# Kernel optimization log

Hardware: AMD Instinct MI355X
Metric: run time of the kernel (lower is better)

## Reference

```python
import jax, jax.numpy as jnp
import numpy as np

RANGE_MIN = -5.0
RANGE_MAX = 5.0
MIN_BIN_SIZE = 1e-4
MIN_SLOPE = 1e-4
N = 33554432  # 32M elements, memory-bound
K = 8         # number of bins -> params has 3*K + 1 = 25 entries


def setup_inputs() -> dict:
    key = jax.random.key(0)
    kx, kp = jax.random.split(key)
    x = jax.random.normal(kx, (N,), dtype=jnp.float32)
    params = jax.random.normal(kp, (3 * K + 1,), dtype=jnp.float32)
    return {"x": x, "params": params}


def _normalize_params(params):
    k = (params.shape[-1] - 1) // 3
    widths_unnorm = params[:k]
    heights_unnorm = params[k:2 * k]
    slopes_unnorm = params[2 * k:]
    total_size = RANGE_MAX - RANGE_MIN
    widths = jax.nn.softmax(widths_unnorm, axis=-1) * (total_size - k * MIN_BIN_SIZE) + MIN_BIN_SIZE
    heights = jax.nn.softmax(heights_unnorm, axis=-1) * (total_size - k * MIN_BIN_SIZE) + MIN_BIN_SIZE
    slopes_offset = jnp.log(jnp.exp(1.0 - MIN_SLOPE) - 1.0)
    slopes = jax.nn.softplus(slopes_unnorm + slopes_offset) + MIN_SLOPE
    x_pos = jnp.concatenate([jnp.array([0.0], dtype=params.dtype), jnp.cumsum(widths)]) + RANGE_MIN
    y_pos = jnp.concatenate([jnp.array([0.0], dtype=params.dtype), jnp.cumsum(heights)]) + RANGE_MIN
    return x_pos, y_pos, slopes


def reference(x, params):
    x_pos, y_pos, slopes = _normalize_params(params)
    below_range = x < RANGE_MIN
    above_range = x > RANGE_MAX
    slope_left, slope_right = slopes[0], slopes[-1]
    y_linear_left = (x - RANGE_MIN) * slope_left + RANGE_MIN
    y_linear_right = (x - RANGE_MAX) * slope_right + RANGE_MAX
    logdet_linear_left = jnp.log(slope_left)
    logdet_linear_right = jnp.log(slope_right)

    num_bins = x_pos.shape[-1] - 1
    bin_idx = jnp.searchsorted(x_pos[1:-1], x, side='right')
    bin_idx = jnp.clip(bin_idx, 0, num_bins - 1)
    x_k, x_k1 = x_pos[bin_idx], x_pos[bin_idx + 1]
    y_k, y_k1 = y_pos[bin_idx], y_pos[bin_idx + 1]
    slope_k, slope_k1 = slopes[bin_idx], slopes[bin_idx + 1]

    width = x_k1 - x_k
    height = y_k1 - y_k
    xi = jnp.clip((x - x_k) / width, 0.0, 1.0)
    s = height / width
    numerator = s * xi * xi + slope_k * xi * (1.0 - xi)
    denominator = s + (slope_k1 + slope_k - 2.0 * s) * xi * (1.0 - xi)
    y_spline = y_k + height * numerator / denominator

    xi_1m = 1.0 - xi
    xi_xi_1m = xi * xi_1m
    num_derivative = s * s * (slope_k1 * xi * xi + 2.0 * s * xi_xi_1m + slope_k * xi_1m * xi_1m)
    derivative = num_derivative / (denominator * denominator)
    logdet_spline = jnp.log(derivative)

    y = jnp.where(below_range, y_linear_left, jnp.where(above_range, y_linear_right, y_spline))
    logdet = jnp.where(below_range, logdet_linear_left, jnp.where(above_range, logdet_linear_right, logdet_spline))
    return (y, logdet)
```

## Files before the change

kernel.cpp:

```cpp
#include <hip/hip_runtime.h>
#include <math.h>

#define KBINS 8
#define R_MIN -5.0f
#define R_MAX 5.0f
#define MIN_BIN 1e-4f
#define MIN_SLOPE 1e-4f


__global__ void rqs_params_kernel(const float* __restrict__ p, float* __restrict__ ws) {
    if (threadIdx.x != 0 || blockIdx.x != 0) return;
    float w[KBINS], h[KBINS], sl[KBINS + 1];
    const float scale = (R_MAX - R_MIN) - KBINS * MIN_BIN;

    float m = -1e30f;
    for (int i = 0; i < KBINS; ++i) m = fmaxf(m, p[i]);
    float sum = 0.f;
    for (int i = 0; i < KBINS; ++i) { w[i] = expf(p[i] - m); sum += w[i]; }
    for (int i = 0; i < KBINS; ++i) w[i] = w[i] / sum * scale + MIN_BIN;

    m = -1e30f;
    for (int i = 0; i < KBINS; ++i) m = fmaxf(m, p[KBINS + i]);
    sum = 0.f;
    for (int i = 0; i < KBINS; ++i) { h[i] = expf(p[KBINS + i] - m); sum += h[i]; }
    for (int i = 0; i < KBINS; ++i) h[i] = h[i] / sum * scale + MIN_BIN;

    const float off = logf(expf(1.0f - MIN_SLOPE) - 1.0f);
    for (int i = 0; i <= KBINS; ++i) {
        float z = p[2 * KBINS + i] + off;
        float sp = (z > 20.f) ? z : log1pf(expf(z));
        sl[i] = sp + MIN_SLOPE;
    }

    float xp[KBINS + 1], yp[KBINS + 1];
    xp[0] = R_MIN; yp[0] = R_MIN;
    for (int i = 0; i < KBINS; ++i) { xp[i + 1] = xp[i] + w[i]; yp[i + 1] = yp[i] + h[i]; }

    for (int i = 0; i <= KBINS; ++i) {
        ws[i] = xp[i];
        ws[9 + i] = yp[i];
        ws[18 + i] = sl[i];
    }
    for (int b = 0; b < KBINS; ++b) {
        float width  = xp[b + 1] - xp[b];
        float height = yp[b + 1] - yp[b];
        float* q = ws + 28 + b * 8;
        q[0] = xp[b];
        q[1] = 1.0f / width;
        q[2] = yp[b];
        q[3] = height;
        q[4] = height / width;
        q[5] = sl[b];
        q[6] = sl[b + 1];
        q[7] = 0.f;
    }
    ws[92] = logf(sl[0]);
    ws[93] = logf(sl[KBINS]);
}

__global__ __launch_bounds__(256) void rqs_main_kernel(
        const float4* __restrict__ x4,
        const float*  __restrict__ ws,
        float4* __restrict__ y4,
        float4* __restrict__ ld4,
        int n4) {
    __shared__ float4 sbin[2 * KBINS];

    const int tid = threadIdx.x;
    if (tid < 2 * KBINS) sbin[tid] = ((const float4*)(ws + 28))[tid];
    __syncthreads();

    const int i = blockIdx.x * blockDim.x + tid;
    if (i >= n4) return;

    const float e1 = ws[1], e2 = ws[2], e3 = ws[3], e4 = ws[4],
                e5 = ws[5], e6 = ws[6], e7 = ws[7];
    const float sl0 = ws[18], slK = ws[26];
    const float lsl0 = ws[92], lslK = ws[93];

    const float4 xv = x4[i];
    const float xs[4] = {xv.x, xv.y, xv.z, xv.w};
    float ys[4], lds_[4];

    #pragma unroll
    for (int j = 0; j < 4; ++j) {
        const float x = xs[j];
        int b = (int)(x >= e1) + (int)(x >= e2) + (int)(x >= e3) + (int)(x >= e4)
              + (int)(x >= e5) + (int)(x >= e6) + (int)(x >= e7);

        const float4 q0 = sbin[2 * b];
        const float4 q1 = sbin[2 * b + 1];

        float xi = (x - q0.x) * q0.y;
        xi = fminf(fmaxf(xi, 0.f), 1.f);
        const float s = q1.x, sk = q1.y, sk1 = q1.z;
        const float xi1m = 1.f - xi;
        const float xx = xi * xi1m;
        const float num  = s * xi * xi + sk * xx;
        const float den  = s + (sk1 + sk - 2.f * s) * xx;
        const float invd = 1.f / den;
        float y = q0.z + q0.w * num * invd;
        const float dnum  = s * s * (sk1 * xi * xi + 2.f * s * xx + sk * xi1m * xi1m);
        const float deriv = dnum * invd * invd;
        float ld = __logf(deriv);

        const bool below = x < R_MIN;
        const bool above = x > R_MAX;
        const float yl = (x - R_MIN) * sl0 + R_MIN;
        const float yr = (x - R_MAX) * slK + R_MAX;
        y  = above ? yr  : y;
        y  = below ? yl  : y;
        ld = above ? lslK : ld;
        ld = below ? lsl0 : ld;

        ys[j] = y;
        lds_[j] = ld;
    }

    y4[i]  = make_float4(ys[0], ys[1], ys[2], ys[3]);
    ld4[i] = make_float4(lds_[0], lds_[1], lds_[2], lds_[3]);
}

extern "C" void kernel_launch(void* const* d_in, const int* in_sizes, int n_in,
                              void* d_out, int out_size, void* d_ws, size_t ws_size,
                              hipStream_t stream) {
    const float* x = (const float*)d_in[0];
    const float* p = (const float*)d_in[1];
    float* out = (float*)d_out;
    float* ws  = (float*)d_ws;
    const int N = in_sizes[0];
    const int n4 = N / 4;

    rqs_params_kernel<<<1, 64, 0, stream>>>(p, ws);
    rqs_main_kernel<<<(n4 + 255) / 256, 256, 0, stream>>>(
        (const float4*)x, ws, (float4*)out, (float4*)out + n4, n4);
}
```

Baseline: 355.7 us.

## Process two float4 per thread with nontemporal stores and padded bin table

Each thread now loads two float4 inputs up front and processes both, halving the block count and exposing more memory-level parallelism per thread. Outputs are written with nontemporal stores to avoid polluting the cache for streaming data. The per-bin LDS table is padded to a 12-float stride, presumably to reduce bank conflicts on the data-dependent gathers. The reciprocal becomes the hardware rcp intrinsic, which is slightly less precise.

New measurement: 371.7 us. +4.5%, slower.

```diff
diff --git a/kernel.cpp b/kernel.cpp
--- a/kernel.cpp
+++ b/kernel.cpp
@@ -6,6 +6,8 @@
 #define R_MAX 5.0f
 #define MIN_BIN 1e-4f
 #define MIN_SLOPE 1e-4f
+
+typedef float v4f __attribute__((ext_vector_type(4)));
 
 
 __global__ void rqs_params_kernel(const float* __restrict__ p, float* __restrict__ ws) {
@@ -44,7 +46,7 @@
     for (int b = 0; b < KBINS; ++b) {
         float width  = xp[b + 1] - xp[b];
         float height = yp[b + 1] - yp[b];
-        float* q = ws + 28 + b * 8;
+        float* q = ws + 28 + b * 12;
         q[0] = xp[b];
         q[1] = 1.0f / width;
         q[2] = yp[b];
@@ -52,73 +54,100 @@
         q[4] = height / width;
         q[5] = sl[b];
         q[6] = sl[b + 1];
-        q[7] = 0.f;
+        q[7] = 0.f; q[8] = 0.f; q[9] = 0.f; q[10] = 0.f; q[11] = 0.f;
     }
-    ws[92] = logf(sl[0]);
-    ws[93] = logf(sl[KBINS]);
+    ws[124] = logf(sl[0]);
+    ws[125] = logf(sl[KBINS]);
+}
+
+__device__ __forceinline__ void rqs_elem(
+        float x, const float* __restrict__ sbin,
+        float e1, float e2, float e3, float e4, float e5, float e6, float e7,
+        float sl0, float slK, float lsl0, float lslK,
+        float& y_out, float& ld_out) {
+    int b = (int)(x >= e1) + (int)(x >= e2) + (int)(x >= e3) + (int)(x >= e4)
+          + (int)(x >= e5) + (int)(x >= e6) + (int)(x >= e7);
+
+    const float* q = sbin + b * 12;
+    const v4f q0 = *(const v4f*)q;
+    const v4f q1 = *(const v4f*)(q + 4);
+
+    float xi = (x - q0[0]) * q0[1];
+    xi = fminf(fmaxf(xi, 0.f), 1.f);
+    const float s = q1[0], sk = q1[1], sk1 = q1[2];
+    const float xi1m = 1.f - xi;
+    const float xx = xi * xi1m;
+    const float num  = s * xi * xi + sk * xx;
+    const float den  = s + (sk1 + sk - 2.f * s) * xx;
+    const float invd = __builtin_amdgcn_rcpf(den);
+    float y = q0[2] + q0[3] * num * invd;
+    const float dnum  = s * s * (sk1 * xi * xi + 2.f * s * xx + sk * xi1m * xi1m);
+    const float deriv = dnum * invd * invd;
+    float ld = __logf(deriv);
+
+    const bool below = x < R_MIN;
+    const bool above = x > R_MAX;
+    const float yl = (x - R_MIN) * sl0 + R_MIN;
+    const float yr = (x - R_MAX) * slK + R_MAX;
+    y  = above ? yr  : y;
+    y  = below ? yl  : y;
+    ld = above ? lslK : ld;
+    ld = below ? lsl0 : ld;
+
+    y_out = y;
+    ld_out = ld;
 }
 
 __global__ __launch_bounds__(256) void rqs_main_kernel(
-        const float4* __restrict__ x4,
+        const v4f* __restrict__ x4,
         const float*  __restrict__ ws,
-        float4* __restrict__ y4,
-        float4* __restrict__ ld4,
+        v4f* __restrict__ y4,
+        v4f* __restrict__ ld4,
         int n4) {
-    __shared__ float4 sbin[2 * KBINS];
+    __shared__ __align__(16) float sbin[KBINS * 12];
 
     const int tid = threadIdx.x;
-    if (tid < 2 * KBINS) sbin[tid] = ((const float4*)(ws + 28))[tid];
+    if (tid < 2 * KBINS + 8) ((v4f*)sbin)[tid] = ((const v4f*)(ws + 28))[tid];
     __syncthreads();
-
-    const int i = blockIdx.x * blockDim.x + tid;
-    if (i >= n4) return;
 
     const float e1 = ws[1], e2 = ws[2], e3 = ws[3], e4 = ws[4],
                 e5 = ws[5], e6 = ws[6], e7 = ws[7];
     const float sl0 = ws[18], slK = ws[26];
-    const float lsl0 = ws[92], lslK = ws[93];
+    const float lsl0 = ws[124], lslK = ws[125];
 
-    const float4 xv = x4[i];
-    const float xs[4] = {xv.x, xv.y, xv.z, xv.w};
-    float ys[4], lds_[4];
+    const int i0 = blockIdx.x * 512 + tid;
+    const int i1 = i0 + 256;
+    const bool has0 = i0 < n4;
+    const bool has1 = i1 < n4;
 
-    #pragma unroll
-    for (int j = 0; j < 4; ++j) {
-        const float x = xs[j];
-        int b = (int)(x >= e1) + (int)(x >= e2) + (int)(x >= e3) + (int)(x >= e4)
-              + (int)(x >= e5) + (int)(x >= e6) + (int)(x >= e7);
+    v4f xv0, xv1;
+    if (has0) xv0 = x4[i0];
+    if (has1) xv1 = x4[i1];
 
-        const float4 q0 = sbin[2 * b];
-        const float4 q1 = sbin[2 * b + 1];
-
-        float xi = (x - q0.x) * q0.y;
-        xi = fminf(fmaxf(xi, 0.f), 1.f);
-        const float s = q1.x, sk = q1.y, sk1 = q1.z;
-        const float xi1m = 1.f - xi;
-        const float xx = xi * xi1m;
-        const float num  = s * xi * xi + sk * xx;
-        const float den  = s + (sk1 + sk - 2.f * s) * xx;
-        const float invd = 1.f / den;
-        float y = q0.z + q0.w * num * invd;
-        const float dnum  = s * s * (sk1 * xi * xi + 2.f * s * xx + sk * xi1m * xi1m);
-        const float deriv = dnum * invd * invd;
-        float ld = __logf(deriv);
-
-        const bool below = x < R_MIN;
-        const bool above = x > R_MAX;
-        const float yl = (x - R_MIN) * sl0 + R_MIN;
-        const float yr = (x - R_MAX) * slK + R_MAX;
-        y  = above ? yr  : y;
-        y  = below ? yl  : y;
-        ld = above ? lslK : ld;
-        ld = below ? lsl0 : ld;
-
-        ys[j] = y;
-        lds_[j] = ld;
+    if (has0) {
+        v4f yv, lv;
+        #pragma unroll
+        for (int j = 0; j < 4; ++j) {
+            float yt, lt;
+            rqs_elem(xv0[j], sbin, e1, e2, e3, e4, e5, e6, e7,
+                     sl0, slK, lsl0, lslK, yt, lt);
+            yv[j] = yt; lv[j] = lt;
+        }
+        __builtin_nontemporal_store(yv, &y4[i0]);
+        __builtin_nontemporal_store(lv, &ld4[i0]);
     }
-
-    y4[i]  = make_float4(ys[0], ys[1], ys[2], ys[3]);
-    ld4[i] = make_float4(lds_[0], lds_[1], lds_[2], lds_[3]);
+    if (has1) {
+        v4f yv, lv;
+        #pragma unroll
+        for (int j = 0; j < 4; ++j) {
+            float yt, lt;
+            rqs_elem(xv1[j], sbin, e1, e2, e3, e4, e5, e6, e7,
+                     sl0, slK, lsl0, lslK, yt, lt);
+            yv[j] = yt; lv[j] = lt;
+        }
+        __builtin_nontemporal_store(yv, &y4[i1]);
+        __builtin_nontemporal_store(lv, &ld4[i1]);
+    }
 }
 
 extern "C" void kernel_launch(void* const* d_in, const int* in_sizes, int n_in,
@@ -132,6 +161,7 @@
     const int n4 = N / 4;
 
     rqs_params_kernel<<<1, 64, 0, stream>>>(p, ws);
-    rqs_main_kernel<<<(n4 + 255) / 256, 256, 0, stream>>>(
-        (const float4*)x, ws, (float4*)out, (float4*)out + n4, n4);
+    const int nblk = (n4 + 511) / 512;
+    rqs_main_kernel<<<nblk, 256, 0, stream>>>(
+        (const v4f*)x, ws, (v4f*)out, (v4f*)out + n4, n4);
 }
```
